# Kernel tuning notes

Hardware: AMD Instinct MI355X
Metric: run time of the kernel (lower is better)

## Reference

```python
import jax, jax.numpy as jnp
import numpy as np

N_DATA = 500000
EMB = 256
K = 4096
BS = 64
T = 0.07
M = 0.5


def _l2norm(x, axis=-1, eps=1e-12):
    return x / jnp.maximum(jnp.linalg.norm(x, axis=axis, keepdims=True), eps)


def setup_inputs() -> dict:
    key = jax.random.key(0)
    k1, k2, k3, k4, k5, k6 = jax.random.split(key, 6)
    vis_feat = jax.random.normal(k1, (BS, EMB), dtype=jnp.float32)
    text_feat = jax.random.normal(k2, (BS, EMB), dtype=jnp.float32)
    # memory banks: original inits uniform in [-stdv, stdv]; randn scaled works the same numerically
    stdv = 1.0 / np.sqrt(EMB / 3)
    vis_memory = jax.random.uniform(k3, (N_DATA, EMB), dtype=jnp.float32, minval=-stdv, maxval=stdv)
    text_memory = jax.random.uniform(k4, (N_DATA, EMB), dtype=jnp.float32, minval=-stdv, maxval=stdv)
    idx = jax.random.randint(k5, (BS,), 0, N_DATA, dtype=jnp.int32)
    slct_idx = jax.random.randint(k6, (BS, K + 1), 0, N_DATA, dtype=jnp.int32)
    # column 0 holds the positive index, as in slct_idx.select(1,0).copy_(idx)
    slct_idx = slct_idx.at[:, 0].set(idx)
    return {
        "vis_feat": vis_feat,
        "text_feat": text_feat,
        "vis_memory": vis_memory,
        "text_memory": text_memory,
        "slct_idx": slct_idx,
        "idx": idx,
    }


def reference(vis_feat, text_feat, vis_memory, text_memory, slct_idx, idx):
    # embeddings are L2-normalized before use (nn.functional.normalize(dim=1))
    vn = _l2norm(vis_feat)   # [bs, D]
    tn = _l2norm(text_feat)  # [bs, D]

    # gather K+1 negatives/positive from memory banks (detached in original)
    tf = jax.lax.stop_gradient(text_memory[slct_idx])  # [bs, K+1, D]
    vf = jax.lax.stop_gradient(vis_memory[slct_idx])   # [bs, K+1, D]

    # batched dot products + exp(./T) (bmm with [bs, D, 1])
    vis_out = jnp.exp(jnp.einsum("bkd,bd->bk", tf, vn) / T)   # [bs, K+1]
    text_out = jnp.exp(jnp.einsum("bkd,bd->bk", vf, tn) / T)  # [bs, K+1]

    # NCE normalization constants, set on first pass: Z = mean * N_data
    Z_v = jax.lax.stop_gradient(jnp.mean(vis_out)) * N_DATA
    Z_t = jax.lax.stop_gradient(jnp.mean(text_out)) * N_DATA
    vis_out = vis_out / Z_v
    text_out = text_out / Z_t

    # EMA memory update + renormalize + scatter (no_grad in original)
    vis_pos = vis_memory[idx] * M + jax.lax.stop_gradient(vn) * (1.0 - M)
    text_pos = text_memory[idx] * M + jax.lax.stop_gradient(tn) * (1.0 - M)
    new_vis_memory = vis_memory.at[idx].set(_l2norm(vis_pos))
    new_text_memory = text_memory.at[idx].set(_l2norm(text_pos))

    return vis_out, text_out, new_vis_memory, new_text_memory
```

## Files before the change

kernel.cpp:

```cpp
#include <hip/hip_runtime.h>

#define NDATA 500000
#define EMB   256
#define BS    64
#define KP1   4097
#define NPAIR (BS * KP1)
#define INV_T (1.0f / 0.07f)

#define SCAN_EPB 2048
#define NB_SCAN  ((NDATA + SCAN_EPB - 1) / SCAN_EPB)
#define RPW      64
#define NBLKF    ((NDATA + RPW * 4 - 1) / (RPW * 4))
#define SCALE_BLKS ((2 * NPAIR + 255) / 256)
#define NBY      17

typedef float    f32x4 __attribute__((ext_vector_type(4)));
typedef unsigned u32x4 __attribute__((ext_vector_type(4)));

__global__ __launch_bounds__(256) void norm_hist_kernel(
    const float* __restrict__ vis_feat, const float* __restrict__ text_feat,
    float* __restrict__ vn, float* __restrict__ tn,
    const int* __restrict__ slct, unsigned* __restrict__ counts,
    unsigned* __restrict__ old) {
  int bid = blockIdx.x;
  if (bid < 128) {
    int b = bid & 63;
    bool is_vis = bid < 64;
    const float* src = (is_vis ? vis_feat : text_feat) + b * EMB;
    float* dst = (is_vis ? vn : tn) + b * EMB;
    int t = threadIdx.x;
    float x = src[t];
    float s = x * x;
    for (int off = 32; off > 0; off >>= 1) s += __shfl_down(s, off, 64);
    __shared__ float red[4];
    if ((t & 63) == 0) red[t >> 6] = s;
    __syncthreads();
    float norm = sqrtf(red[0] + red[1] + red[2] + red[3]);
    dst[t] = x / fmaxf(norm, 1e-12f);
  } else {
    int i = (bid - 128) * 256 + threadIdx.x;
    if (i < NPAIR) {
      int r = slct[i];
      old[i] = atomicAdd(&counts[r], 1u);
    }
  }
}

__global__ __launch_bounds__(256) void scan1_kernel(
    const unsigned* __restrict__ counts, unsigned* __restrict__ start,
    unsigned* __restrict__ bsum) {
  int t = threadIdx.x;
  int base = blockIdx.x * SCAN_EPB + t * 8;
  unsigned v[8];
  unsigned tsum = 0;
#pragma unroll
  for (int j = 0; j < 8; ++j) {
    int i = base + j;
    unsigned c = (i < NDATA) ? counts[i] : 0u;
    v[j] = tsum;
    tsum += c;
  }
  unsigned x = tsum;
  for (int d = 1; d < 64; d <<= 1) {
    unsigned y = __shfl_up(x, d, 64);
    if ((t & 63) >= d) x += y;
  }
  __shared__ unsigned wsum[4];
  if ((t & 63) == 63) wsum[t >> 6] = x;
  __syncthreads();
  unsigned woff = 0;
  for (int wv = 0; wv < (t >> 6); ++wv) woff += wsum[wv];
  unsigned ex = woff + x - tsum;
#pragma unroll
  for (int j = 0; j < 8; ++j) {
    int i = base + j;
    if (i < NDATA) start[i] = ex + v[j];
  }
  if (t == 255) bsum[blockIdx.x] = woff + x;
}

__global__ __launch_bounds__(256) void scan2_kernel(unsigned* __restrict__ bsum) {
  int t = threadIdx.x;
  unsigned v = (t < NB_SCAN) ? bsum[t] : 0u;
  unsigned x = v;
  for (int d = 1; d < 64; d <<= 1) {
    unsigned y = __shfl_up(x, d, 64);
    if ((t & 63) >= d) x += y;
  }
  __shared__ unsigned wsum[4];
  if ((t & 63) == 63) wsum[t >> 6] = x;
  __syncthreads();
  unsigned woff = 0;
  for (int wv = 0; wv < (t >> 6); ++wv) woff += wsum[wv];
  unsigned ex = woff + x - v;
  if (t < NB_SCAN) bsum[t] = ex;
}

__global__ __launch_bounds__(256) void scatter_kernel(
    const int* __restrict__ slct, const unsigned* __restrict__ start,
    const unsigned* __restrict__ bsum, const unsigned* __restrict__ old,
    unsigned* __restrict__ pairs) {
  int i = blockIdx.x * 256 + threadIdx.x;
  if (i < NPAIR) {
    int r = slct[i];
    unsigned pos = start[r] + bsum[r >> 11] + old[i];
    int b = i / KP1;
    int kk = i - b * KP1;
    pairs[pos] = ((unsigned)b << 13) | (unsigned)kk;
  }
}

#define LOADC(R, rb)                                                          \
  { _Pragma("unroll") for (int j = 0; j < 8; ++j)                             \
      R[j] = __builtin_nontemporal_load(&s4[(size_t)((rb) + j) * 64 + lane]); }

#define STOREC(R, rb)                                                         \
  { _Pragma("unroll") for (int j = 0; j < 8; ++j)                             \
      __builtin_nontemporal_store(R[j], &d4[(size_t)((rb) + j) * 64 + lane]); }

#define REFS(R, rb)                                                           \
  { u32x4 c0 = *(const u32x4*)&counts[(rb)];                                  \
    u32x4 c1 = *(const u32x4*)&counts[(rb) + 4];                              \
    u32x4 s0 = *(const u32x4*)&start[(rb)];                                   \
    u32x4 s1 = *(const u32x4*)&start[(rb) + 4];                               \
    unsigned cn[8] = {c0.x, c0.y, c0.z, c0.w, c1.x, c1.y, c1.z, c1.w};        \
    unsigned sn[8] = {s0.x, s0.y, s0.z, s0.w, s1.x, s1.y, s1.z, s1.w};        \
    _Pragma("unroll") for (int j = 0; j < 8; ++j) {                           \
      unsigned n = cn[j];                                                     \
      if (n) {                                                                \
        unsigned gs = sn[j] + bs;                                             \
        for (unsigned u = 0; u < n; ++u) {                                    \
          unsigned p = pairs[gs + u];                                         \
          int bb = (int)(p >> 13), kk = (int)(p & 8191u);                     \
          f32x4 fv = f4[bb * 64 + lane];                                      \
          float d = R[j].x * fv.x + R[j].y * fv.y + R[j].z * fv.z + R[j].w * fv.w; \
          for (int off = 32; off > 0; off >>= 1) d += __shfl_down(d, off, 64);\
          if (lane == 0) {                                                    \
            float e = __expf(d * INV_T);                                      \
            outz[bb * KP1 + kk] = e;                                          \
            local += e;                                                       \
          }                                                                   \
        }                                                                     \
      }                                                                       \
    } }

__global__ __launch_bounds__(256) void fused_copy_dot_kernel(
    const float* __restrict__ text_mem, const float* __restrict__ vis_mem,
    float* __restrict__ out_text, float* __restrict__ out_vis,
    const float* __restrict__ vn, const float* __restrict__ tn,
    const unsigned* __restrict__ counts, const unsigned* __restrict__ start,
    const unsigned* __restrict__ bsum, const unsigned* __restrict__ pairs,
    float* __restrict__ out, float* __restrict__ partials) {
  int z = blockIdx.z;
  const f32x4* s4 = (const f32x4*)(z == 0 ? text_mem : vis_mem);
  f32x4* d4 = (f32x4*)(z == 0 ? out_text : out_vis);
  const f32x4* f4 = (const f32x4*)(z == 0 ? vn : tn);
  float* outz = out + (size_t)z * NPAIR;

  int t = threadIdx.x, w = t >> 6, lane = t & 63;
  int gw = blockIdx.x * 4 + w;
  int r0 = gw * RPW;
  float local = 0.f;

  if (r0 < NDATA) {
    int rend = min(r0 + RPW, NDATA);
    int nch = (rend - r0) >> 3;
    unsigned bs = bsum[r0 >> 11];
    f32x4 A[8], B[8];
    int rb = r0, c = 0;
    LOADC(A, rb);
    while (true) {
      if (c + 1 < nch) LOADC(B, rb + 8);
      STOREC(A, rb);
      REFS(A, rb);
      ++c; rb += 8; if (c >= nch) break;
      if (c + 1 < nch) LOADC(A, rb + 8);
      STOREC(B, rb);
      REFS(B, rb);
      ++c; rb += 8; if (c >= nch) break;
    }
  }
  __shared__ float red[4];
  if (lane == 0) red[w] = local;
  __syncthreads();
  if (t == 0)
    partials[(size_t)z * NBLKF + blockIdx.x] = red[0] + red[1] + red[2] + red[3];
}

__global__ __launch_bounds__(256) void reduce_z_kernel(
    const float* __restrict__ partials, float* __restrict__ zsum, int per_z) {
  int z = blockIdx.x;
  const float* p = partials + (size_t)z * per_z;
  float s = 0.f;
  for (int i = threadIdx.x; i < per_z; i += 256) s += p[i];
  for (int off = 32; off > 0; off >>= 1) s += __shfl_down(s, off, 64);
  __shared__ float red[4];
  if ((threadIdx.x & 63) == 0) red[threadIdx.x >> 6] = s;
  __syncthreads();
  if (threadIdx.x == 0) zsum[z] = red[0] + red[1] + red[2] + red[3];
}

__global__ __launch_bounds__(256) void scale_update_kernel(
    float* __restrict__ out, const float* __restrict__ zsum,
    const float* __restrict__ vis_mem, const float* __restrict__ text_mem,
    const float* __restrict__ vn, const float* __restrict__ tn,
    const int* __restrict__ idx,
    float* __restrict__ out_vis, float* __restrict__ out_text) {
  int bid = blockIdx.x;
  if (bid < SCALE_BLKS) {
    int i = bid * 256 + threadIdx.x;
    if (i < 2 * NPAIR) {
      float Z = ((i < NPAIR) ? zsum[0] : zsum[1]) * ((float)NDATA / (float)NPAIR);
      out[i] = out[i] / Z;
    }
  } else {
    int bb = bid - SCALE_BLKS;
    int b = bb & 63;
    bool is_vis = bb < 64;
    int row = idx[b];
    for (int b2 = b + 1; b2 < BS; ++b2)
      if (idx[b2] == row) return;
    const float* mem  = (is_vis ? vis_mem : text_mem) + (size_t)row * EMB;
    const float* feat = (is_vis ? vn : tn) + b * EMB;
    float* dst = (is_vis ? out_vis : out_text) + (size_t)row * EMB;
    int t = threadIdx.x;
    float p = mem[t] * 0.5f + feat[t] * 0.5f;
    float s = p * p;
    for (int off = 32; off > 0; off >>= 1) s += __shfl_down(s, off, 64);
    __shared__ float red[4];
    if ((t & 63) == 0) red[t >> 6] = s;
    __syncthreads();
    float norm = sqrtf(red[0] + red[1] + red[2] + red[3]);
    dst[t] = p / fmaxf(norm, 1e-12f);
  }
}

__global__ __launch_bounds__(256) void dot_exp_kernel(
    const float* __restrict__ text_mem, const float* __restrict__ vis_mem,
    const float* __restrict__ vn, const float* __restrict__ tn,
    const int* __restrict__ slct, float* __restrict__ out,
    float* __restrict__ partials) {
  int b = blockIdx.x;
  int z = blockIdx.z;
  const float* mem  = (z == 0) ? text_mem : vis_mem;
  const float* feat = (z == 0) ? vn : tn;
  float* o = out + (size_t)z * NPAIR + (size_t)b * KP1;
  const int* srow = slct + b * KP1;
  __shared__ float4 sf[64];
  int t = threadIdx.x;
  if (t < 64) sf[t] = ((const float4*)(feat + b * EMB))[t];
  __syncthreads();
  int w = t >> 6, lane = t & 63;
  float4 f = sf[lane];
  int kbase = blockIdx.y * 256 + w * 64;
  int kend  = min(kbase + 64, KP1);
  float local = 0.f;
  int k = kbase;
  for (; k + 2 <= kend; k += 2) {
    int r0 = srow[k], r1 = srow[k + 1];
    float4 v0 = ((const float4*)(mem + (size_t)r0 * EMB))[lane];
    float4 v1 = ((const float4*)(mem + (size_t)r1 * EMB))[lane];
    float p0 = v0.x * f.x + v0.y * f.y + v0.z * f.z + v0.w * f.w;
    float p1 = v1.x * f.x + v1.y * f.y + v1.z * f.z + v1.w * f.w;
    for (int off = 32; off > 0; off >>= 1) {
      p0 += __shfl_down(p0, off, 64);
      p1 += __shfl_down(p1, off, 64);
    }
    if (lane == 0) {
      float e0 = __expf(p0 * INV_T);
      float e1 = __expf(p1 * INV_T);
      o[k] = e0; o[k + 1] = e1;
      local += e0 + e1;
    }
  }
  if (k < kend) {
    int r0 = srow[k];
    float4 v0 = ((const float4*)(mem + (size_t)r0 * EMB))[lane];
    float p0 = v0.x * f.x + v0.y * f.y + v0.z * f.z + v0.w * f.w;
    for (int off = 32; off > 0; off >>= 1) p0 += __shfl_down(p0, off, 64);
    if (lane == 0) { float e0 = __expf(p0 * INV_T); o[k] = e0; local += e0; }
  }
  __shared__ float red[4];
  if (lane == 0) red[w] = local;
  __syncthreads();
  if (t == 0)
    partials[((size_t)z * NBY + blockIdx.y) * BS + b] =
        red[0] + red[1] + red[2] + red[3];
}

__global__ __launch_bounds__(256) void copy2_kernel(
    const float4* __restrict__ src_a, float4* __restrict__ dst_a,
    const float4* __restrict__ src_b, float4* __restrict__ dst_b, long n4) {
  long i = (long)blockIdx.x * blockDim.x + threadIdx.x;
  long stride = (long)gridDim.x * blockDim.x;
  for (; i < 2 * n4; i += stride) {
    if (i < n4) dst_a[i] = src_a[i];
    else        dst_b[i - n4] = src_b[i - n4];
  }
}

extern "C" void kernel_launch(void* const* d_in, const int* in_sizes, int n_in,
                              void* d_out, int out_size, void* d_ws, size_t ws_size,
                              hipStream_t stream) {
  const float* vis_feat  = (const float*)d_in[0];
  const float* text_feat = (const float*)d_in[1];
  const float* vis_mem   = (const float*)d_in[2];
  const float* text_mem  = (const float*)d_in[3];
  const int*   slct      = (const int*)d_in[4];
  const int*   idx       = (const int*)d_in[5];

  float* out          = (float*)d_out;
  float* out_vis_mem  = out + (size_t)2 * NPAIR;
  float* out_text_mem = out_vis_mem + (size_t)NDATA * EMB;

  float*    ws       = (float*)d_ws;
  float*    vn       = ws;
  float*    tn       = vn + BS * EMB;
  float*    zsum     = tn + BS * EMB;
  float*    partials = zsum + 4;
  unsigned* counts   = (unsigned*)(partials + 2 * NBLKF);
  unsigned* start    = counts + NDATA;
  unsigned* bsum     = start + NDATA;
  unsigned* old      = bsum + 256;
  unsigned* pairs    = old + NPAIR;
  size_t needed = ((size_t)(2 * BS * EMB + 4 + 2 * NBLKF) +
                   (size_t)(2 * NDATA + 256 + 2 * NPAIR)) * 4;

  if (ws_size >= needed) {
    hipMemsetAsync(counts, 0, NDATA * sizeof(unsigned), stream);
    norm_hist_kernel<<<128 + (NPAIR + 255) / 256, 256, 0, stream>>>(
        vis_feat, text_feat, vn, tn, slct, counts, old);
    scan1_kernel<<<NB_SCAN, 256, 0, stream>>>(counts, start, bsum);
    scan2_kernel<<<1, 256, 0, stream>>>(bsum);
    scatter_kernel<<<(NPAIR + 255) / 256, 256, 0, stream>>>(slct, start, bsum, old, pairs);

    dim3 gF(NBLKF, 1, 2);
    fused_copy_dot_kernel<<<gF, 256, 0, stream>>>(
        text_mem, vis_mem, out_text_mem, out_vis_mem, vn, tn,
        counts, start, bsum, pairs, out, partials);

    reduce_z_kernel<<<2, 256, 0, stream>>>(partials, zsum, NBLKF);
  } else {
    norm_hist_kernel<<<128, 256, 0, stream>>>(
        vis_feat, text_feat, vn, tn, slct, counts, old);
    dim3 gB(BS, NBY, 2);
    dot_exp_kernel<<<gB, 256, 0, stream>>>(text_mem, vis_mem, vn, tn, slct, out,
                                           partials);
    reduce_z_kernel<<<2, 256, 0, stream>>>(partials, zsum, NBY * BS);
    const long n4 = (long)NDATA * EMB / 4;
    copy2_kernel<<<8192, 256, 0, stream>>>(
        (const float4*)vis_mem,  (float4*)out_vis_mem,
        (const float4*)text_mem, (float4*)out_text_mem, n4);
  }

  scale_update_kernel<<<SCALE_BLKS + 128, 256, 0, stream>>>(
      out, zsum, vis_mem, text_mem, vn, tn, idx, out_vis_mem, out_text_mem);
}
```

Baseline: 458.9 us.

## Halve rows per wave, prefetch pair gathers, atomically accumulate Z sums

Each wave of the fused copy+dot kernel now handles 32 rows instead of 64, as a fully unrolled four-chunk load/store schedule, doubling the number of waves for more parallelism. The inner reference loop software-prefetches the next pair index and feature vector so gather latency overlaps the dot product and reduction. The separate reduce_z kernel launch is replaced by per-block atomicAdd into a zeroed zsum, saving a launch at the cost of many contended atomics and a nondeterministic summation order. The workspace is reordered so one memset clears both zsum and counts.

```diff
diff --git a/kernel.cpp b/kernel.cpp
--- a/kernel.cpp
+++ b/kernel.cpp
@@ -9,8 +9,9 @@
 
 #define SCAN_EPB 2048
 #define NB_SCAN  ((NDATA + SCAN_EPB - 1) / SCAN_EPB)
-#define RPW      64
-#define NBLKF    ((NDATA + RPW * 4 - 1) / (RPW * 4))
+#define RPW      32
+#define NWAVES   (NDATA / RPW)
+#define NBLKF    ((NWAVES + 3) / 4)
 #define SCALE_BLKS ((2 * NPAIR + 255) / 256)
 #define NBY      17
 
@@ -129,17 +130,22 @@
       unsigned n = cn[j];                                                     \
       if (n) {                                                                \
         unsigned gs = sn[j] + bs;                                             \
+        unsigned p = pairs[gs];                                               \
+        f32x4 fv = f4[(p >> 13) * 64 + lane];                                 \
         for (unsigned u = 0; u < n; ++u) {                                    \
-          unsigned p = pairs[gs + u];                                         \
-          int bb = (int)(p >> 13), kk = (int)(p & 8191u);                     \
-          f32x4 fv = f4[bb * 64 + lane];                                      \
+          unsigned pn = p; f32x4 fvn = fv;                                    \
+          if (u + 1 < n) {                                                    \
+            pn = pairs[gs + u + 1];                                           \
+            fvn = f4[(pn >> 13) * 64 + lane];                                 \
+          }                                                                   \
           float d = R[j].x * fv.x + R[j].y * fv.y + R[j].z * fv.z + R[j].w * fv.w; \
           for (int off = 32; off > 0; off >>= 1) d += __shfl_down(d, off, 64);\
           if (lane == 0) {                                                    \
             float e = __expf(d * INV_T);                                      \
-            outz[bb * KP1 + kk] = e;                                          \
+            outz[(p >> 13) * KP1 + (p & 8191u)] = e;                          \
             local += e;                                                       \
           }                                                                   \
+          p = pn; fv = fvn;                                                   \
         }                                                                     \
       }                                                                       \
     } }
@@ -150,7 +156,7 @@
     const float* __restrict__ vn, const float* __restrict__ tn,
     const unsigned* __restrict__ counts, const unsigned* __restrict__ start,
     const unsigned* __restrict__ bsum, const unsigned* __restrict__ pairs,
-    float* __restrict__ out, float* __restrict__ partials) {
+    float* __restrict__ out, float* __restrict__ zsum) {
   int z = blockIdx.z;
   const f32x4* s4 = (const f32x4*)(z == 0 ? text_mem : vis_mem);
   f32x4* d4 = (f32x4*)(z == 0 ? out_text : out_vis);
@@ -159,45 +165,28 @@
 
   int t = threadIdx.x, w = t >> 6, lane = t & 63;
   int gw = blockIdx.x * 4 + w;
-  int r0 = gw * RPW;
   float local = 0.f;
 
-  if (r0 < NDATA) {
-    int rend = min(r0 + RPW, NDATA);
-    int nch = (rend - r0) >> 3;
+  if (gw < NWAVES) {
+    int r0 = gw * RPW;
     unsigned bs = bsum[r0 >> 11];
     f32x4 A[8], B[8];
-    int rb = r0, c = 0;
-    LOADC(A, rb);
-    while (true) {
-      if (c + 1 < nch) LOADC(B, rb + 8);
-      STOREC(A, rb);
-      REFS(A, rb);
-      ++c; rb += 8; if (c >= nch) break;
-      if (c + 1 < nch) LOADC(A, rb + 8);
-      STOREC(B, rb);
-      REFS(B, rb);
-      ++c; rb += 8; if (c >= nch) break;
-    }
+    LOADC(A, r0);
+    LOADC(B, r0 + 8);
+    STOREC(A, r0);      REFS(A, r0);
+    LOADC(A, r0 + 16);
+    STOREC(B, r0 + 8);  REFS(B, r0 + 8);
+    LOADC(B, r0 + 24);
+    STOREC(A, r0 + 16); REFS(A, r0 + 16);
+    STOREC(B, r0 + 24); REFS(B, r0 + 24);
   }
   __shared__ float red[4];
   if (lane == 0) red[w] = local;
   __syncthreads();
-  if (t == 0)
-    partials[(size_t)z * NBLKF + blockIdx.x] = red[0] + red[1] + red[2] + red[3];
-}
-
-__global__ __launch_bounds__(256) void reduce_z_kernel(
-    const float* __restrict__ partials, float* __restrict__ zsum, int per_z) {
-  int z = blockIdx.x;
-  const float* p = partials + (size_t)z * per_z;
-  float s = 0.f;
-  for (int i = threadIdx.x; i < per_z; i += 256) s += p[i];
-  for (int off = 32; off > 0; off >>= 1) s += __shfl_down(s, off, 64);
-  __shared__ float red[4];
-  if ((threadIdx.x & 63) == 0) red[threadIdx.x >> 6] = s;
-  __syncthreads();
-  if (threadIdx.x == 0) zsum[z] = red[0] + red[1] + red[2] + red[3];
+  if (t == 0) {
+    float s = red[0] + red[1] + red[2] + red[3];
+    atomicAdd(&zsum[z], s);
+  }
 }
 
 __global__ __launch_bounds__(256) void scale_update_kernel(
@@ -288,6 +277,19 @@
         red[0] + red[1] + red[2] + red[3];
 }
 
+__global__ __launch_bounds__(256) void reduce_z_kernel(
+    const float* __restrict__ partials, float* __restrict__ zsum, int per_z) {
+  int z = blockIdx.x;
+  const float* p = partials + (size_t)z * per_z;
+  float s = 0.f;
+  for (int i = threadIdx.x; i < per_z; i += 256) s += p[i];
+  for (int off = 32; off > 0; off >>= 1) s += __shfl_down(s, off, 64);
+  __shared__ float red[4];
+  if ((threadIdx.x & 63) == 0) red[threadIdx.x >> 6] = s;
+  __syncthreads();
+  if (threadIdx.x == 0) zsum[z] = red[0] + red[1] + red[2] + red[3];
+}
+
 __global__ __launch_bounds__(256) void copy2_kernel(
     const float4* __restrict__ src_a, float4* __restrict__ dst_a,
     const float4* __restrict__ src_b, float4* __restrict__ dst_b, long n4) {
@@ -313,21 +315,20 @@
   float* out_vis_mem  = out + (size_t)2 * NPAIR;
   float* out_text_mem = out_vis_mem + (size_t)NDATA * EMB;
 
-  float*    ws       = (float*)d_ws;
-  float*    vn       = ws;
-  float*    tn       = vn + BS * EMB;
-  float*    zsum     = tn + BS * EMB;
-  float*    partials = zsum + 4;
-  unsigned* counts   = (unsigned*)(partials + 2 * NBLKF);
-  unsigned* start    = counts + NDATA;
-  unsigned* bsum     = start + NDATA;
-  unsigned* old      = bsum + 256;
-  unsigned* pairs    = old + NPAIR;
-  size_t needed = ((size_t)(2 * BS * EMB + 4 + 2 * NBLKF) +
-                   (size_t)(2 * NDATA + 256 + 2 * NPAIR)) * 4;
+  float*    ws     = (float*)d_ws;
+  float*    zsum   = ws;
+  unsigned* counts = (unsigned*)(zsum + 4);
+  unsigned* start  = counts + NDATA;
+  unsigned* bsum   = start + NDATA;
+  unsigned* old    = bsum + 256;
+  unsigned* pairs  = old + NPAIR;
+  float*    vn     = (float*)(pairs + NPAIR);
+  float*    tn     = vn + BS * EMB;
+  size_t needed = ((size_t)(4 + 2 * NDATA + 256 + 2 * NPAIR) +
+                   (size_t)(2 * BS * EMB)) * 4;
 
   if (ws_size >= needed) {
-    hipMemsetAsync(counts, 0, NDATA * sizeof(unsigned), stream);
+    hipMemsetAsync(zsum, 0, (4 + NDATA) * sizeof(unsigned), stream);
     norm_hist_kernel<<<128 + (NPAIR + 255) / 256, 256, 0, stream>>>(
         vis_feat, text_feat, vn, tn, slct, counts, old);
     scan1_kernel<<<NB_SCAN, 256, 0, stream>>>(counts, start, bsum);
@@ -337,16 +338,14 @@
     dim3 gF(NBLKF, 1, 2);
     fused_copy_dot_kernel<<<gF, 256, 0, stream>>>(
         text_mem, vis_mem, out_text_mem, out_vis_mem, vn, tn,
-        counts, start, bsum, pairs, out, partials);
-
-    reduce_z_kernel<<<2, 256, 0, stream>>>(partials, zsum, NBLKF);
+        counts, start, bsum, pairs, out, zsum);
   } else {
     norm_hist_kernel<<<128, 256, 0, stream>>>(
         vis_feat, text_feat, vn, tn, slct, counts, old);
     dim3 gB(BS, NBY, 2);
     dot_exp_kernel<<<gB, 256, 0, stream>>>(text_mem, vis_mem, vn, tn, slct, out,
-                                           partials);
-    reduce_z_kernel<<<2, 256, 0, stream>>>(partials, zsum, NBY * BS);
+                                           (float*)old);
+    reduce_z_kernel<<<2, 256, 0, stream>>>((float*)old, zsum, NBY * BS);
     const long n4 = (long)NDATA * EMB / 4;
     copy2_kernel<<<8192, 256, 0, stream>>>(
         (const float4*)vis_mem,  (float4*)out_vis_mem,
```

New measurement: 432.5 us. -5.8%, faster.
